# Kernel tuning notes

Measured on AMD Instinct MI355X. Metric: run time of the kernel, lower is better.

## Reference

```python
import jax, jax.numpy as jnp
import numpy as np

FS = 100
KERNEL = FS * 3 + 1  # 301, matches nn.AvgPool1d(kernel_size, stride=1, padding=K//2, count_include_pad=True)


def _avg_pool1d(x, k):
    # x: [B, L] -> same-length moving average with zero padding counted in the divisor
    w = jnp.full((1, 1, k), 1.0 / k, dtype=x.dtype)
    y = jax.lax.conv_general_dilated(
        x[:, None, :], w, window_strides=(1,), padding=[(k // 2, k // 2)],
        dimension_numbers=("NCH", "OIH", "NCH"))
    return y[:, 0, :]


def _unwrap_phase(phase):
    # torch-faithful np.unwrap: [B, L]
    d = jnp.diff(phase, axis=-1)
    dm = jnp.mod(d + jnp.pi, 2.0 * jnp.pi) - jnp.pi
    dm = jnp.where((dm == -jnp.pi) & (d > 0), jnp.pi, dm)
    offset = jnp.cumsum(d - dm, axis=-1)
    unwrapped = jnp.concatenate([phase[..., :1], phase[..., 1:] + offset], axis=-1)
    return jnp.nan_to_num(unwrapped, nan=0.0)


def _normalize(x):
    # zero mean, unit (unbiased, like torch.std) variance along last dim
    n = x.shape[-1]
    mean = jnp.mean(x, axis=-1, keepdims=True)
    var = jnp.sum((x - mean) ** 2, axis=-1, keepdims=True) / (n - 1)
    return (x - mean) / (jnp.sqrt(var) + 1e-5)


def setup_inputs() -> dict:
    key = jax.random.key(0)
    k1, k2 = jax.random.split(key)
    B, L = 64, 262144
    return {
        "radar_i": jax.random.normal(k1, (B, L), dtype=jnp.float32),
        "radar_q": jax.random.normal(k2, (B, L), dtype=jnp.float32),
    }


def reference(radar_i, radar_q):
    magnitude = jnp.nan_to_num(jnp.sqrt(radar_i ** 2 + radar_q ** 2), nan=0.0)
    phase = jnp.nan_to_num(jnp.arctan2(radar_q, radar_i), nan=0.0)
    phase_unwrap = _unwrap_phase(phase)
    phase_filt = phase_unwrap - _avg_pool1d(phase_unwrap, KERNEL)
    magnitude_filt = magnitude - _avg_pool1d(magnitude, KERNEL)
    magnitude_norm = jnp.nan_to_num(_normalize(magnitude_filt), nan=0.0)
    phase_norm = jnp.nan_to_num(_normalize(phase_filt), nan=0.0)
    return jnp.stack([magnitude_norm, phase_norm], axis=1)  # [B, 2, L]
```

## Files before the change

kernel.cpp:

```cpp
#include <hip/hip_runtime.h>
#include <math.h>

#define TPB 256
constexpr int Bn = 64;
constexpr int Ln = 262144;
constexpr int S  = 4096;
constexpr int NC = Ln / S;
constexpr int HA = S + 301;
constexpr int EPT = 18;
constexpr int HAP = EPT * TPB;
constexpr int OPT = S / TPB;
constexpr int A4 = 4400;
constexpr int NV4 = A4 / 4;
constexpr int LDSZ = 4624;

constexpr float TWO_PI_F = 6.28318530717958647692f;
constexpr float PI_F = 3.14159265358979323846f;
constexpr float HALF_PI_F = 1.57079632679489661923f;
constexpr float INV_TWO_PI_F = 0.15915494309189533577f;

__device__ __forceinline__ int wrap_k(float d) {
    float kf = floorf(__fmaf_rn(d, INV_TWO_PI_F, 0.5f));
    float dm = __fmaf_rn(-kf, TWO_PI_F, d);
    if (dm == -PI_F && d > 0.f) kf -= 1.f;
    return (int)kf;
}

__device__ __forceinline__ float fast_atan2f(float q, float i) {
    float aq = fabsf(q), ai = fabsf(i);
    float mx = fmaxf(aq, ai), mn = fminf(aq, ai);
    float r = __builtin_amdgcn_rcpf(mx);
    r = r * (2.0f - mx * r);
    float t = mn * r;
    if (mx == 0.f) t = 0.f;
    float s = t * t;
    float p = __fmaf_rn(s, 0.0028662257f, -0.0161657367f);
    p = __fmaf_rn(p, s,  0.0429096138f);
    p = __fmaf_rn(p, s, -0.0752896400f);
    p = __fmaf_rn(p, s,  0.1065626393f);
    p = __fmaf_rn(p, s, -0.1420889944f);
    p = __fmaf_rn(p, s,  0.1999355085f);
    p = __fmaf_rn(p, s, -0.3333314528f);
    float at = __fmaf_rn(p * s, t, t);
    if (aq > ai) at = HALF_PI_F - at;
    if (i < 0.f) at = PI_F - at;
    return (q < 0.f) ? -at : at;
}

__device__ __forceinline__ int wave_iscan_int(int v) {
    int lane = threadIdx.x & 63;
#pragma unroll
    for (int o = 1; o < 64; o <<= 1) {
        int u = __shfl_up(v, o, 64);
        if (lane >= o) v += u;
    }
    return v;
}

__device__ __forceinline__ int block_escan_int(int v, int* wtot) {
    int tid = threadIdx.x, wid = tid >> 6, lane = tid & 63;
    int inc = wave_iscan_int(v);
    __syncthreads();
    if (lane == 63) wtot[wid] = inc;
    __syncthreads();
    int add = 0;
#pragma unroll
    for (int w = 0; w < TPB / 64; ++w) add += (w < wid) ? wtot[w] : 0;
    return inc - v + add;
}

__device__ __forceinline__ double block_escan_double(double v, double* wtot) {
    int tid = threadIdx.x, wid = tid >> 6, lane = tid & 63;
    double inc = v;
#pragma unroll
    for (int o = 1; o < 64; o <<= 1) {
        double u = __shfl_up(inc, o, 64);
        if (lane >= o) inc += u;
    }
    __syncthreads();
    if (lane == 63) wtot[wid] = inc;
    __syncthreads();
    double add = 0.0;
#pragma unroll
    for (int w = 0; w < TPB / 64; ++w) add += (w < wid) ? wtot[w] : 0.0;
    return inc - v + add;
}

__global__ __launch_bounds__(TPB, 4) void k_filt(const float* __restrict__ Ig,
                                                 const float* __restrict__ Qg,
                                                 int* __restrict__ Ag,
                                                 int* __restrict__ Bg,
                                                 float* __restrict__ out,
                                                 double* __restrict__ PS) {
    __shared__ __align__(16) float spu_s[LDSZ];
    __shared__ __align__(16) float smg_s[LDSZ];
    __shared__ int iw[TPB / 64];
    __shared__ double dw[TPB / 64];
    __shared__ double rbuf[TPB / 64][4];
    float* spu = spu_s + 1;
    float* smg = smg_s + 1;

    const int c = blockIdx.x, b = blockIdx.y;
    const int t0 = c * S;
    const int base = t0 - 151;
    const int tid = threadIdx.x;
    const float* Ib = Ig + (size_t)b * Ln;
    const float* Qb = Qg + (size_t)b * Ln;

    if (c > 0 && c < NC - 1) {
        const int astart = base - 1;
        const float4* I4 = reinterpret_cast<const float4*>(Ib + astart);
        const float4* Q4 = reinterpret_cast<const float4*>(Qb + astart);
        float4 vi[5], vq[5];
#pragma unroll
        for (int j = 0; j < 5; ++j) {
            int k = tid + j * TPB;
            if (k < NV4) { vi[j] = I4[k]; vq[j] = Q4[k]; }
        }
        if (tid < LDSZ - A4) { spu_s[A4 + tid] = 0.f; smg_s[A4 + tid] = 0.f; }
#pragma unroll
        for (int j = 0; j < 5; ++j) {
            int k = tid + j * TPB;
            if (k < NV4) {
                float4 vp, vm;
                vm.x = sqrtf(__fmaf_rn(vi[j].x, vi[j].x, vq[j].x * vq[j].x));
                vm.y = sqrtf(__fmaf_rn(vi[j].y, vi[j].y, vq[j].y * vq[j].y));
                vm.z = sqrtf(__fmaf_rn(vi[j].z, vi[j].z, vq[j].z * vq[j].z));
                vm.w = sqrtf(__fmaf_rn(vi[j].w, vi[j].w, vq[j].w * vq[j].w));
                vp.x = fast_atan2f(vq[j].x, vi[j].x);
                vp.y = fast_atan2f(vq[j].y, vi[j].y);
                vp.z = fast_atan2f(vq[j].z, vi[j].z);
                vp.w = fast_atan2f(vq[j].w, vi[j].w);
                reinterpret_cast<float4*>(spu_s)[k] = vp;
                reinterpret_cast<float4*>(smg_s)[k] = vm;
            }
        }
    } else {
#pragma unroll
        for (int j = 0; j < EPT; ++j) {
            int li = tid + j * TPB;
            int g = base + li;
            float ph = 0.f, m = 0.f;
            if (li < HA && g >= 0 && g < Ln) {
                float iv = Ib[g], qv = Qb[g];
                m = sqrtf(__fmaf_rn(iv, iv, qv * qv));
                ph = fast_atan2f(qv, iv);
            }
            spu[li] = ph;
            smg[li] = m;
        }
    }
    __syncthreads();

    const int seg = tid * EPT;

    float ph[EPT];
    int kloc[EPT];
    {
        float prev = (seg > 0) ? spu[seg - 1] : 0.f;
        int run = 0;
#pragma unroll
        for (int i = 0; i < EPT; ++i) {
            float cur = spu[seg + i];
            ph[i] = cur;
            int k = wrap_k(cur - prev);
            if (seg + i == 0) k = 0;
            run += k;
            kloc[i] = run;
            prev = cur;
        }
    }
    const int excl = block_escan_int(kloc[EPT - 1], iw);
    if (tid == 8)   Ag[b * NC + c] = excl + kloc[6];
    if (tid == 235) Bg[b * NC + c] = excl + kloc[16];

#pragma unroll
    for (int i = 0; i < EPT; ++i) {
        int li = seg + i;
        int g = base + li;
        float pu = 0.f;
        if (li < HA && g >= 0 && g < Ln)
            pu = ph[i] + (float)(excl + kloc[i]) * TWO_PI_F;
        spu[li] = pu;
    }
    __syncthreads();

    float xp[OPT], xm[OPT];
#pragma unroll
    for (int j = 0; j < OPT; ++j) {
        int lt = tid + j * TPB + 151;
        xp[j] = spu[lt];
        xm[j] = smg[lt];
    }

    float rp = 0.f, rm = 0.f;
#pragma unroll
    for (int i = 0; i < EPT; ++i) {
        rp += spu[seg + i];
        rm += smg[seg + i];
    }
    double ep = block_escan_double((double)rp, dw);
    double em = block_escan_double((double)rm, dw);

    {
        double runp = ep, runm = em;
#pragma unroll
        for (int i = 0; i < EPT; ++i) {
            int li = seg + i;
            runp += (double)spu[li];
            spu[li] = (float)runp;
            runm += (double)smg[li];
            smg[li] = (float)runm;
        }
    }
    __syncthreads();

    float s1mf = 0.f, s2mf = 0.f, s1pf = 0.f, s2pf = 0.f;
    float* om = out + ((size_t)b * 2) * Ln + t0;
    float* op = out + ((size_t)b * 2 + 1) * Ln + t0;
    constexpr float INV_K = 1.0f / 301.0f;
#pragma unroll
    for (int j = 0; j < OPT; ++j) {
        int t = tid + j * TPB;
        int lt = t + 151;
        float am = (smg[lt + 150] - smg[lt - 151]) * INV_K;
        float fm = xm[j] - am;
        float ap = (spu[lt + 150] - spu[lt - 151]) * INV_K;
        float fp = xp[j] - ap;
        om[t] = fm;
        op[t] = fp;
        s1mf += fm; s2mf = __fmaf_rn(fm, fm, s2mf);
        s1pf += fp; s2pf = __fmaf_rn(fp, fp, s2pf);
    }
    double a0 = (double)s1mf, a1 = (double)s2mf, a2 = (double)s1pf, a3 = (double)s2pf;
    int lane = tid & 63, wid = tid >> 6;
#pragma unroll
    for (int o = 32; o > 0; o >>= 1) {
        a0 += __shfl_down(a0, o, 64);
        a1 += __shfl_down(a1, o, 64);
        a2 += __shfl_down(a2, o, 64);
        a3 += __shfl_down(a3, o, 64);
    }
    if (lane == 0) { rbuf[wid][0] = a0; rbuf[wid][1] = a1; rbuf[wid][2] = a2; rbuf[wid][3] = a3; }
    __syncthreads();
    if (tid == 0) {
        double t0d = 0, t1d = 0, t2d = 0, t3d = 0;
#pragma unroll
        for (int w = 0; w < TPB / 64; ++w) {
            t0d += rbuf[w][0]; t1d += rbuf[w][1]; t2d += rbuf[w][2]; t3d += rbuf[w][3];
        }
        double* p = PS + (size_t)(b * NC + c) * 4;
        p[0] = t0d; p[1] = t1d; p[2] = t2d; p[3] = t3d;
    }
}

__global__ void k_fix(const int* __restrict__ Ag, const int* __restrict__ Bg,
                      float* __restrict__ out, double* __restrict__ PS) {
    const int b = blockIdx.x;
    const int lane = threadIdx.x;
    int a = Ag[b * NC + lane];
    int bb = Bg[b * NC + lane];
    int a63 = __shfl(a, 63, 64);
    int w = (lane < 63) ? (bb - a) : 0;
#pragma unroll
    for (int o = 32; o > 0; o >>= 1) w += __shfl_down(w, o, 64);
    int O63 = __shfl(w, 0, 64);
    float C = TWO_PI_F * (float)(O63 - a63);

    constexpr float INV_K = 1.0f / 301.0f;
    float* op = out + ((size_t)b * 2 + 1) * Ln;
    double sd = 0.0, sd2 = 0.0;
#pragma unroll
    for (int k = 0; k < 3; ++k) {
        int j = lane + k * 64;
        if (j < 150) {
            int t = Ln - 150 + j;
            float delta = C * (float)(j + 1) * INV_K;
            float v = op[t];
            float nv = v + delta;
            op[t] = nv;
            sd += (double)delta;
            sd2 += (double)nv * (double)nv - (double)v * (double)v;
        }
    }
#pragma unroll
    for (int o = 32; o > 0; o >>= 1) {
        sd += __shfl_down(sd, o, 64);
        sd2 += __shfl_down(sd2, o, 64);
    }
    if (lane == 0) {
        double* p = PS + (size_t)(b * NC + 63) * 4;
        p[2] += sd;
        p[3] += sd2;
    }
}

__global__ void k_stats(const double* __restrict__ PS, float* __restrict__ ROW) {
    int b = blockIdx.x;
    const double* p = PS + (size_t)(b * NC + threadIdx.x) * 4;
    double a0 = p[0], a1 = p[1], a2 = p[2], a3 = p[3];
#pragma unroll
    for (int o = 32; o > 0; o >>= 1) {
        a0 += __shfl_down(a0, o, 64);
        a1 += __shfl_down(a1, o, 64);
        a2 += __shfl_down(a2, o, 64);
        a3 += __shfl_down(a3, o, 64);
    }
    if (threadIdx.x == 0) {
        double Ld = (double)Ln;
        double mm = a0 / Ld;
        double vm = (a1 - a0 * a0 / Ld) / (Ld - 1.0); vm = vm > 0 ? vm : 0;
        double mp = a2 / Ld;
        double vp = (a3 - a2 * a2 / Ld) / (Ld - 1.0); vp = vp > 0 ? vp : 0;
        float* r = ROW + b * 4;
        r[0] = (float)mm;
        r[1] = (float)(1.0 / (sqrt(vm) + 1e-5));
        r[2] = (float)mp;
        r[3] = (float)(1.0 / (sqrt(vp) + 1e-5));
    }
}

__global__ __launch_bounds__(TPB) void k_norm(float* __restrict__ out,
                                              const float* __restrict__ ROW) {
    const size_t n4 = (size_t)Bn * 2 * Ln / 4;
    size_t stride = (size_t)gridDim.x * blockDim.x;
    for (size_t p4 = (size_t)blockIdx.x * blockDim.x + threadIdx.x; p4 < n4; p4 += stride) {
        size_t p = p4 * 4;
        int b = (int)(p >> 19);
        int sig = (int)((p >> 18) & 1);
        float mean = ROW[b * 4 + sig * 2];
        float scale = ROW[b * 4 + sig * 2 + 1];
        float4 v = reinterpret_cast<float4*>(out)[p4];
        v.x = (v.x - mean) * scale;
        v.y = (v.y - mean) * scale;
        v.z = (v.z - mean) * scale;
        v.w = (v.w - mean) * scale;
        reinterpret_cast<float4*>(out)[p4] = v;
    }
}

extern "C" void kernel_launch(void* const* d_in, const int* in_sizes, int n_in,
                              void* d_out, int out_size, void* d_ws, size_t ws_size,
                              hipStream_t stream) {
    const float* Ig = (const float*)d_in[0];
    const float* Qg = (const float*)d_in[1];
    float* out = (float*)d_out;
    char* ws = (char*)d_ws;
    int* Ag = (int*)ws;
    int* Bg = (int*)(ws + 16384);
    double* PS = (double*)(ws + 32768);
    float* ROW = (float*)(ws + 32768 + (size_t)Bn * NC * 4 * sizeof(double));

    dim3 grid(NC, Bn);
    hipLaunchKernelGGL(k_filt, grid, dim3(TPB), 0, stream, Ig, Qg, Ag, Bg, out, PS);
    hipLaunchKernelGGL(k_fix, dim3(Bn), dim3(64), 0, stream, Ag, Bg, out, PS);
    hipLaunchKernelGGL(k_stats, dim3(Bn), dim3(64), 0, stream, PS, ROW);
    hipLaunchKernelGGL(k_norm, dim3(2048), dim3(TPB), 0, stream, out, ROW);
}
```

Measured before the change: 118.7 us.

## Halve chunk size, switch prefix scans to float, fuse fix and stats kernels

Chunk size per block drops from 4096 to 2048 samples with 10 elements per thread and occupancy hint 6, and loads become float2. The integer wrap scan and the magnitude sum scan now share one pass, and the running prefix sums move from double to float using values kept in registers. The k_fix and k_stats kernels merge into one k_post kernel that reads float partial stats. The aim is fewer double-precision ops, fewer barriers and launches, and more parallel blocks, at the cost of more halo overhead per chunk and lower precision in the prefix sums.

```diff
diff --git a/kernel.cpp b/kernel.cpp
--- a/kernel.cpp
+++ b/kernel.cpp
@@ -4,15 +4,15 @@
 #define TPB 256
 constexpr int Bn = 64;
 constexpr int Ln = 262144;
-constexpr int S  = 4096;
+constexpr int S  = 2048;
 constexpr int NC = Ln / S;
 constexpr int HA = S + 301;
-constexpr int EPT = 18;
+constexpr int EPT = 10;
 constexpr int HAP = EPT * TPB;
 constexpr int OPT = S / TPB;
-constexpr int A4 = 4400;
-constexpr int NV4 = A4 / 4;
-constexpr int LDSZ = 4624;
+constexpr int A4 = 2352;
+constexpr int NP = A4 / 2;
+constexpr int LDSZ = 2564;
 
 constexpr float TWO_PI_F = 6.28318530717958647692f;
 constexpr float PI_F = 3.14159265358979323846f;
@@ -47,55 +47,16 @@
     return (q < 0.f) ? -at : at;
 }
 
-__device__ __forceinline__ int wave_iscan_int(int v) {
-    int lane = threadIdx.x & 63;
-#pragma unroll
-    for (int o = 1; o < 64; o <<= 1) {
-        int u = __shfl_up(v, o, 64);
-        if (lane >= o) v += u;
-    }
-    return v;
-}
-
-__device__ __forceinline__ int block_escan_int(int v, int* wtot) {
-    int tid = threadIdx.x, wid = tid >> 6, lane = tid & 63;
-    int inc = wave_iscan_int(v);
-    __syncthreads();
-    if (lane == 63) wtot[wid] = inc;
-    __syncthreads();
-    int add = 0;
-#pragma unroll
-    for (int w = 0; w < TPB / 64; ++w) add += (w < wid) ? wtot[w] : 0;
-    return inc - v + add;
-}
-
-__device__ __forceinline__ double block_escan_double(double v, double* wtot) {
-    int tid = threadIdx.x, wid = tid >> 6, lane = tid & 63;
-    double inc = v;
-#pragma unroll
-    for (int o = 1; o < 64; o <<= 1) {
-        double u = __shfl_up(inc, o, 64);
-        if (lane >= o) inc += u;
-    }
-    __syncthreads();
-    if (lane == 63) wtot[wid] = inc;
-    __syncthreads();
-    double add = 0.0;
-#pragma unroll
-    for (int w = 0; w < TPB / 64; ++w) add += (w < wid) ? wtot[w] : 0.0;
-    return inc - v + add;
-}
-
-__global__ __launch_bounds__(TPB, 4) void k_filt(const float* __restrict__ Ig,
+__global__ __launch_bounds__(TPB, 6) void k_filt(const float* __restrict__ Ig,
                                                  const float* __restrict__ Qg,
                                                  int* __restrict__ Ag,
                                                  int* __restrict__ Bg,
                                                  float* __restrict__ out,
-                                                 double* __restrict__ PS) {
+                                                 float* __restrict__ PS) {
     __shared__ __align__(16) float spu_s[LDSZ];
     __shared__ __align__(16) float smg_s[LDSZ];
-    __shared__ int iw[TPB / 64];
-    __shared__ double dw[TPB / 64];
+    __shared__ int iwt[TPB / 64];
+    __shared__ float fwt[TPB / 64];
     __shared__ double rbuf[TPB / 64][4];
     float* spu = spu_s + 1;
     float* smg = smg_s + 1;
@@ -104,35 +65,29 @@
     const int t0 = c * S;
     const int base = t0 - 151;
     const int tid = threadIdx.x;
+    const int lane = tid & 63, wid = tid >> 6;
     const float* Ib = Ig + (size_t)b * Ln;
     const float* Qb = Qg + (size_t)b * Ln;
 
     if (c > 0 && c < NC - 1) {
         const int astart = base - 1;
-        const float4* I4 = reinterpret_cast<const float4*>(Ib + astart);
-        const float4* Q4 = reinterpret_cast<const float4*>(Qb + astart);
-        float4 vi[5], vq[5];
+        const float2* I2 = reinterpret_cast<const float2*>(Ib + astart);
+        const float2* Q2 = reinterpret_cast<const float2*>(Qb + astart);
+        if (tid < LDSZ - A4) { spu_s[A4 + tid] = 0.f; smg_s[A4 + tid] = 0.f; }
+        float2 vi[5], vq[5];
 #pragma unroll
         for (int j = 0; j < 5; ++j) {
-            int k = tid + j * TPB;
-            if (k < NV4) { vi[j] = I4[k]; vq[j] = Q4[k]; }
-        }
-        if (tid < LDSZ - A4) { spu_s[A4 + tid] = 0.f; smg_s[A4 + tid] = 0.f; }
+            int p = tid + j * TPB;
+            if (p < NP) { vi[j] = I2[p]; vq[j] = Q2[p]; }
+        }
 #pragma unroll
         for (int j = 0; j < 5; ++j) {
-            int k = tid + j * TPB;
-            if (k < NV4) {
-                float4 vp, vm;
-                vm.x = sqrtf(__fmaf_rn(vi[j].x, vi[j].x, vq[j].x * vq[j].x));
-                vm.y = sqrtf(__fmaf_rn(vi[j].y, vi[j].y, vq[j].y * vq[j].y));
-                vm.z = sqrtf(__fmaf_rn(vi[j].z, vi[j].z, vq[j].z * vq[j].z));
-                vm.w = sqrtf(__fmaf_rn(vi[j].w, vi[j].w, vq[j].w * vq[j].w));
-                vp.x = fast_atan2f(vq[j].x, vi[j].x);
-                vp.y = fast_atan2f(vq[j].y, vi[j].y);
-                vp.z = fast_atan2f(vq[j].z, vi[j].z);
-                vp.w = fast_atan2f(vq[j].w, vi[j].w);
-                reinterpret_cast<float4*>(spu_s)[k] = vp;
-                reinterpret_cast<float4*>(smg_s)[k] = vm;
+            int p = tid + j * TPB;
+            if (p < NP) {
+                spu_s[2 * p]     = fast_atan2f(vq[j].x, vi[j].x);
+                spu_s[2 * p + 1] = fast_atan2f(vq[j].y, vi[j].y);
+                smg_s[2 * p]     = sqrtf(__fmaf_rn(vi[j].x, vi[j].x, vq[j].x * vq[j].x));
+                smg_s[2 * p + 1] = sqrtf(__fmaf_rn(vi[j].y, vi[j].y, vq[j].y * vq[j].y));
             }
         }
     } else {
@@ -154,37 +109,68 @@
 
     const int seg = tid * EPT;
 
-    float ph[EPT];
+    float ph[EPT], mg[EPT];
     int kloc[EPT];
+    float rm = 0.f;
     {
         float prev = (seg > 0) ? spu[seg - 1] : 0.f;
         int run = 0;
 #pragma unroll
         for (int i = 0; i < EPT; ++i) {
-            float cur = spu[seg + i];
-            ph[i] = cur;
-            int k = wrap_k(cur - prev);
-            if (seg + i == 0) k = 0;
-            run += k;
+            ph[i] = spu[seg + i];
+            mg[i] = smg[seg + i];
+            run += wrap_k(ph[i] - prev);
             kloc[i] = run;
-            prev = cur;
-        }
-    }
-    const int excl = block_escan_int(kloc[EPT - 1], iw);
-    if (tid == 8)   Ag[b * NC + c] = excl + kloc[6];
-    if (tid == 235) Bg[b * NC + c] = excl + kloc[16];
-
+            prev = ph[i];
+            rm += mg[i];
+        }
+    }
+
+    int vi_ = kloc[EPT - 1];
+    float vf = rm;
+#pragma unroll
+    for (int o = 1; o < 64; o <<= 1) {
+        int ui = __shfl_up(vi_, o, 64);
+        float uf = __shfl_up(vf, o, 64);
+        if (lane >= o) { vi_ += ui; vf += uf; }
+    }
+    __syncthreads();
+    if (lane == 63) { iwt[wid] = vi_; fwt[wid] = vf; }
+    __syncthreads();
+    int addi = 0; float addf = 0.f;
+#pragma unroll
+    for (int w = 0; w < TPB / 64; ++w) {
+        addi += (w < wid) ? iwt[w] : 0;
+        addf += (w < wid) ? fwt[w] : 0.f;
+    }
+    const int excl = vi_ - kloc[EPT - 1] + addi;
+    const float em = vf - rm + addf;
+
+    if (tid == 15)  Ag[b * NC + c] = excl + kloc[0];
+    if (tid == 219) Bg[b * NC + c] = excl + kloc[8];
+
+    float pu[EPT];
+    float rp = 0.f;
 #pragma unroll
     for (int i = 0; i < EPT; ++i) {
         int li = seg + i;
         int g = base + li;
-        float pu = 0.f;
+        float v = 0.f;
         if (li < HA && g >= 0 && g < Ln)
-            pu = ph[i] + (float)(excl + kloc[i]) * TWO_PI_F;
-        spu[li] = pu;
-    }
-    __syncthreads();
-
+            v = ph[i] + (float)(excl + kloc[i]) * TWO_PI_F;
+        pu[i] = v;
+        rp += v;
+        spu[li] = v;
+    }
+
+    float incf = rp;
+#pragma unroll
+    for (int o = 1; o < 64; o <<= 1) {
+        float uf = __shfl_up(incf, o, 64);
+        if (lane >= o) incf += uf;
+    }
+    __syncthreads();
+    if (lane == 63) fwt[wid] = incf;
     float xp[OPT], xm[OPT];
 #pragma unroll
     for (int j = 0; j < OPT; ++j) {
@@ -192,25 +178,21 @@
         xp[j] = spu[lt];
         xm[j] = smg[lt];
     }
-
-    float rp = 0.f, rm = 0.f;
-#pragma unroll
-    for (int i = 0; i < EPT; ++i) {
-        rp += spu[seg + i];
-        rm += smg[seg + i];
-    }
-    double ep = block_escan_double((double)rp, dw);
-    double em = block_escan_double((double)rm, dw);
+    __syncthreads();
+    float addp = 0.f;
+#pragma unroll
+    for (int w = 0; w < TPB / 64; ++w) addp += (w < wid) ? fwt[w] : 0.f;
+    const float ep = incf - rp + addp;
 
     {
-        double runp = ep, runm = em;
+        float runp = ep, runm = em;
 #pragma unroll
         for (int i = 0; i < EPT; ++i) {
             int li = seg + i;
-            runp += (double)spu[li];
-            spu[li] = (float)runp;
-            runm += (double)smg[li];
-            smg[li] = (float)runm;
+            runp += pu[i];
+            spu[li] = runp;
+            runm += mg[i];
+            smg[li] = runm;
         }
     }
     __syncthreads();
@@ -233,7 +215,6 @@
         s1pf += fp; s2pf = __fmaf_rn(fp, fp, s2pf);
     }
     double a0 = (double)s1mf, a1 = (double)s2mf, a2 = (double)s1pf, a3 = (double)s2pf;
-    int lane = tid & 63, wid = tid >> 6;
 #pragma unroll
     for (int o = 32; o > 0; o >>= 1) {
         a0 += __shfl_down(a0, o, 64);
@@ -249,23 +230,25 @@
         for (int w = 0; w < TPB / 64; ++w) {
             t0d += rbuf[w][0]; t1d += rbuf[w][1]; t2d += rbuf[w][2]; t3d += rbuf[w][3];
         }
-        double* p = PS + (size_t)(b * NC + c) * 4;
-        p[0] = t0d; p[1] = t1d; p[2] = t2d; p[3] = t3d;
-    }
-}
-
-__global__ void k_fix(const int* __restrict__ Ag, const int* __restrict__ Bg,
-                      float* __restrict__ out, double* __restrict__ PS) {
+        float* p = PS + (size_t)(b * NC + c) * 4;
+        p[0] = (float)t0d; p[1] = (float)t1d; p[2] = (float)t2d; p[3] = (float)t3d;
+    }
+}
+
+__global__ void k_post(const int* __restrict__ Ag, const int* __restrict__ Bg,
+                       float* __restrict__ out, const float* __restrict__ PS,
+                       float* __restrict__ ROW) {
     const int b = blockIdx.x;
     const int lane = threadIdx.x;
-    int a = Ag[b * NC + lane];
-    int bb = Bg[b * NC + lane];
-    int a63 = __shfl(a, 63, 64);
-    int w = (lane < 63) ? (bb - a) : 0;
+    const int idx = b * NC;
+
+    int w = (Bg[idx + lane] - Ag[idx + lane]);
+    if (lane + 64 < NC - 1) w += (Bg[idx + 64 + lane] - Ag[idx + 64 + lane]);
 #pragma unroll
     for (int o = 32; o > 0; o >>= 1) w += __shfl_down(w, o, 64);
-    int O63 = __shfl(w, 0, 64);
-    float C = TWO_PI_F * (float)(O63 - a63);
+    int O = __shfl(w, 0, 64);
+    int aL = Ag[idx + NC - 1];
+    float C = TWO_PI_F * (float)(O - aL);
 
     constexpr float INV_K = 1.0f / 301.0f;
     float* op = out + ((size_t)b * 2 + 1) * Ln;
@@ -283,22 +266,13 @@
             sd2 += (double)nv * (double)nv - (double)v * (double)v;
         }
     }
-#pragma unroll
-    for (int o = 32; o > 0; o >>= 1) {
-        sd += __shfl_down(sd, o, 64);
-        sd2 += __shfl_down(sd2, o, 64);
-    }
-    if (lane == 0) {
-        double* p = PS + (size_t)(b * NC + 63) * 4;
-        p[2] += sd;
-        p[3] += sd2;
-    }
-}
-
-__global__ void k_stats(const double* __restrict__ PS, float* __restrict__ ROW) {
-    int b = blockIdx.x;
-    const double* p = PS + (size_t)(b * NC + threadIdx.x) * 4;
-    double a0 = p[0], a1 = p[1], a2 = p[2], a3 = p[3];
+
+    const float* p1 = PS + (size_t)(idx + lane) * 4;
+    const float* p2 = PS + (size_t)(idx + 64 + lane) * 4;
+    double a0 = (double)p1[0] + (double)p2[0];
+    double a1 = (double)p1[1] + (double)p2[1];
+    double a2 = (double)p1[2] + (double)p2[2] + sd;
+    double a3 = (double)p1[3] + (double)p2[3] + sd2;
 #pragma unroll
     for (int o = 32; o > 0; o >>= 1) {
         a0 += __shfl_down(a0, o, 64);
@@ -306,7 +280,7 @@
         a2 += __shfl_down(a2, o, 64);
         a3 += __shfl_down(a3, o, 64);
     }
-    if (threadIdx.x == 0) {
+    if (lane == 0) {
         double Ld = (double)Ln;
         double mm = a0 / Ld;
         double vm = (a1 - a0 * a0 / Ld) / (Ld - 1.0); vm = vm > 0 ? vm : 0;
@@ -347,13 +321,12 @@
     float* out = (float*)d_out;
     char* ws = (char*)d_ws;
     int* Ag = (int*)ws;
-    int* Bg = (int*)(ws + 16384);
-    double* PS = (double*)(ws + 32768);
-    float* ROW = (float*)(ws + 32768 + (size_t)Bn * NC * 4 * sizeof(double));
+    int* Bg = (int*)(ws + 32768);
+    float* PS = (float*)(ws + 65536);
+    float* ROW = (float*)(ws + 65536 + (size_t)Bn * NC * 4 * sizeof(float));
 
     dim3 grid(NC, Bn);
     hipLaunchKernelGGL(k_filt, grid, dim3(TPB), 0, stream, Ig, Qg, Ag, Bg, out, PS);
-    hipLaunchKernelGGL(k_fix, dim3(Bn), dim3(64), 0, stream, Ag, Bg, out, PS);
-    hipLaunchKernelGGL(k_stats, dim3(Bn), dim3(64), 0, stream, PS, ROW);
+    hipLaunchKernelGGL(k_post, dim3(Bn), dim3(64), 0, stream, Ag, Bg, out, PS, ROW);
     hipLaunchKernelGGL(k_norm, dim3(2048), dim3(TPB), 0, stream, out, ROW);
 }
```

After: 109.9 us. -7.4%, faster.
